# Kernel optimization log

Measured on AMD Instinct MI355X. Metric: run time of the kernel, lower is better.

## Reference

```python
import jax, jax.numpy as jnp
import numpy as np

N_BATCHES = 32
N_LABELS = 100


def setup_inputs() -> dict:
    key = jax.random.key(0)
    ks = jax.random.split(key, 7)
    N, D, P = 16384, 2048, 256
    x = jax.random.normal(ks[0], (N, D), dtype=jnp.float32)
    label = jax.random.randint(ks[1], (N,), 0, N_LABELS, dtype=jnp.int64)
    label_batch = jnp.sort(jax.random.randint(ks[2], (N,), 0, N_BATCHES, dtype=jnp.int64))
    W1_w = jax.random.normal(ks[3], (P, D), dtype=jnp.float32) * 0.02
    W1_b = jax.random.normal(ks[4], (P,), dtype=jnp.float32) * 0.02
    W2_w = jax.random.normal(ks[5], (P, D), dtype=jnp.float32) * 0.02
    W2_b = jax.random.normal(ks[6], (P,), dtype=jnp.float32) * 0.02
    return {"x": x, "label": label, "label_batch": label_batch,
            "W1_w": W1_w, "W1_b": W1_b, "W2_w": W2_w, "W2_b": W2_b}


def _loo_diff_label_mean(x, label, label_batch):
    # For each sample i: mean of x over {j : label_batch[j]==label_batch[i] and label[j]!=label[i]}.
    # Rows with no such j are zero (torch code's `continue`). x is detached in the original.
    N = x.shape[0]
    xs = jax.lax.stop_gradient(x)
    seg = label_batch * N_LABELS + label                      # combined (group,label) key
    n_seg = N_BATCHES * N_LABELS
    ones = jnp.ones((N,), dtype=x.dtype)
    sum_bl = jax.ops.segment_sum(xs, seg, num_segments=n_seg)            # [n_seg, D]
    cnt_bl = jax.ops.segment_sum(ones, seg, num_segments=n_seg)          # [n_seg]
    sum_b = jax.ops.segment_sum(xs, label_batch, num_segments=N_BATCHES)  # [NB, D]
    cnt_b = jax.ops.segment_sum(ones, label_batch, num_segments=N_BATCHES)
    diff_sum = sum_b[label_batch] - sum_bl[seg]               # [N, D]
    diff_cnt = cnt_b[label_batch] - cnt_bl[seg]               # [N]
    safe = jnp.maximum(diff_cnt, 1.0)
    mean = diff_sum / safe[:, None]
    return jnp.where((diff_cnt > 0)[:, None], mean, jnp.zeros_like(mean))


def reference(x, label, label_batch, W1_w, W1_b, W2_w, W2_b):
    calc_mean = _loo_diff_label_mean(x, label, label_batch)   # detached aggregate
    return x @ W1_w.T + W1_b + calc_mean @ W2_w.T + W2_b      # W1(x) + W2(mean)
```

## Files before the change

### kernel.cpp

```cpp
#include <hip/hip_runtime.h>
#include <cstdint>

#define N_SAMPLES 16384
#define DIM 2048
#define PDIM 256
#define NB 32
#define NL 100
#define NSEG (NB * NL)

typedef float floatx4 __attribute__((ext_vector_type(4)));
typedef __bf16 bf16x8 __attribute__((ext_vector_type(8)));

__device__ __forceinline__ unsigned short f32_to_bf16(float f) {
    unsigned int u = __float_as_uint(f);
    u += 0x7fffu + ((u >> 16) & 1u);
    return (unsigned short)(u >> 16);
}
__device__ __forceinline__ unsigned int pack_bf16x2(float a, float b) {
    return (unsigned int)f32_to_bf16(a) | ((unsigned int)f32_to_bf16(b) << 16);
}

__global__ __launch_bounds__(256) void prep_kernel(
    const float* __restrict__ W1w, const float* __restrict__ W1b,
    const float* __restrict__ W2w, const float* __restrict__ W2b,
    const int* __restrict__ label, const int* __restrict__ lbatch,
    unsigned short* __restrict__ W1bf, unsigned short* __restrict__ W2bf,
    float* __restrict__ bias, int* __restrict__ seg,
    int* __restrict__ hist, float* __restrict__ MW2)
{
    int i = blockIdx.x * 256 + threadIdx.x;
    W1bf[i] = f32_to_bf16(W1w[i]);
    W2bf[i] = f32_to_bf16(W2w[i]);
    if (i < PDIM) bias[i] = W1b[i] + W2b[i];
    if (i < N_SAMPLES) seg[i] = lbatch[i] * NL + label[i];
    if (i < NSEG) hist[i] = 0;
    if (i < NSEG * PDIM / 2) ((float2*)MW2)[i] = make_float2(0.f, 0.f);
}

__global__ __launch_bounds__(256) void hist_kernel(
    const int* __restrict__ seg, int* __restrict__ hist)
{
    int i = blockIdx.x * 256 + threadIdx.x;
    atomicAdd(&hist[seg[i]], 1);
}

#define SCAN_BPT 13
__global__ __launch_bounds__(256) void scan_kernel(
    const int* __restrict__ hist, int* __restrict__ offs, int* __restrict__ cursor)
{
    __shared__ int ps[256];
    const int t = threadIdx.x;
    int local = 0;
    #pragma unroll
    for (int k = 0; k < SCAN_BPT; ++k) {
        int bin = t * SCAN_BPT + k;
        if (bin < NSEG) local += hist[bin];
    }
    ps[t] = local;
    __syncthreads();
    for (int d = 1; d < 256; d <<= 1) {
        int v = (t >= d) ? ps[t - d] : 0;
        __syncthreads();
        ps[t] += v;
        __syncthreads();
    }
    int run = ps[t] - local;
    #pragma unroll
    for (int k = 0; k < SCAN_BPT; ++k) {
        int bin = t * SCAN_BPT + k;
        if (bin < NSEG) {
            offs[bin] = run;
            cursor[bin] = run;
            run += hist[bin];
        }
    }
    if (t == 255) offs[NSEG] = ps[255];
}

__global__ __launch_bounds__(256) void scatter_kernel(
    const int* __restrict__ seg, int* __restrict__ cursor, int* __restrict__ perm)
{
    int i = blockIdx.x * 256 + threadIdx.x;
    int pos = atomicAdd(&cursor[seg[i]], 1);
    perm[pos] = i;
}

__global__ __launch_bounds__(256) void segsum_kernel(
    const float* __restrict__ x, const int* __restrict__ perm,
    const int* __restrict__ offs,
    unsigned short* __restrict__ xb, float* __restrict__ sum_bl)
{
    const int tid = threadIdx.x;
    const int w = tid >> 6, lane = tid & 63;
    const int s = blockIdx.y * 4 + w;
    const int c = blockIdx.x * 512 + lane * 8;
    const int beg = offs[s], end = offs[s + 1];

    floatx4 sum0 = {0.f, 0.f, 0.f, 0.f};
    floatx4 sum1 = {0.f, 0.f, 0.f, 0.f};
    for (int base = beg; base < end; base += 64) {
        int p = (base + lane < end) ? perm[base + lane] : 0;
        const int n = min(end - base, 64);
        for (int j0 = 0; j0 < n; j0 += 8) {
            int rr[8];
            floatx4 v0[8], v1[8];
            #pragma unroll
            for (int j = 0; j < 8; ++j) {
                rr[j] = __shfl(p, min(j0 + j, n - 1));
                const float* px = &x[(size_t)rr[j] * DIM + c];
                v0[j] = *(const floatx4*)px;
                v1[j] = *(const floatx4*)(px + 4);
            }
            #pragma unroll
            for (int j = 0; j < 8; ++j) {
                if (j < n - j0) {
                    sum0 += v0[j];
                    sum1 += v1[j];
                    uint4 o;
                    o.x = pack_bf16x2(v0[j][0], v0[j][1]);
                    o.y = pack_bf16x2(v0[j][2], v0[j][3]);
                    o.z = pack_bf16x2(v1[j][0], v1[j][1]);
                    o.w = pack_bf16x2(v1[j][2], v1[j][3]);
                    *(uint4*)&xb[(size_t)rr[j] * DIM + c] = o;
                }
            }
        }
    }
    *(floatx4*)&sum_bl[(size_t)s * DIM + c] = sum0;
    *(floatx4*)&sum_bl[(size_t)s * DIM + c + 4] = sum1;
}

__global__ __launch_bounds__(256) void meanm_kernel(
    const float* __restrict__ sum_bl, const int* __restrict__ offs,
    unsigned short* __restrict__ Mb)
{
    __shared__ float acc[NL][256];
    const int tid = threadIdx.x;
    const int b = blockIdx.y;
    const int c = blockIdx.x * 256 + tid;

    float tot = 0.f;
    for (int l0 = 0; l0 < NL; l0 += 4) {
        float v[4];
        #pragma unroll
        for (int j = 0; j < 4; ++j)
            v[j] = sum_bl[(size_t)(b * NL + l0 + j) * DIM + c];
        #pragma unroll
        for (int j = 0; j < 4; ++j) { acc[l0 + j][tid] = v[j]; tot += v[j]; }
    }

    const int ob = offs[b * NL];
    const int cb = offs[(b + 1) * NL] - ob;
    for (int l = 0; l < NL; ++l) {
        int dc = cb - (offs[b * NL + l + 1] - offs[b * NL + l]);
        float m = (dc > 0) ? (tot - acc[l][tid]) / (float)dc : 0.f;
        Mb[(size_t)(b * NL + l) * DIM + c] = f32_to_bf16(m);
    }
}

template<int BM, int BN, int WR, int WC, bool FUSE, int KSPLIT>
__global__ __launch_bounds__(256) void gemm_bt_kernel(
    const unsigned short* __restrict__ A,
    const unsigned short* __restrict__ B,
    float* __restrict__ C,
    const float* __restrict__ bias,
    const float* __restrict__ add,
    const int* __restrict__ seg,
    int K)
{
    constexpr int SM = BM / WR, SN = BN / WC;
    constexpr int FM = SM / 16, FN = SN / 16;
    __shared__ __align__(16) unsigned short ldsA[BM * 32];
    __shared__ __align__(16) unsigned short ldsB[BN * 32];
    const int tid = threadIdx.x;
    const int lane = tid & 63;
    const int wave = tid >> 6;
    const int wr = wave / WC, wc = wave % WC;
    const int quad = lane >> 4, l15 = lane & 15;
    const int m0 = blockIdx.x * BM;
    const int n0 = blockIdx.y * BN;
    const int kpw = K / KSPLIT;
    const int k0 = blockIdx.z * kpw;
    const int srow = lane >> 2, schunk = lane & 3;

    floatx4 acc[FM][FN];
    #pragma unroll
    for (int i = 0; i < FM; ++i)
        #pragma unroll
        for (int j = 0; j < FN; ++j) acc[i][j] = (floatx4){0.f, 0.f, 0.f, 0.f};

    const unsigned short* Abase = A + (size_t)(m0 + srow) * K + schunk * 8;
    const unsigned short* Bbase = B + (size_t)(n0 + srow) * K + schunk * 8;

    for (int kk = k0; kk < k0 + kpw; kk += 32) {
        __syncthreads();
        #pragma unroll
        for (int ch = wave; ch < BM / 16; ch += 4)
            __builtin_amdgcn_global_load_lds(
                (const __attribute__((address_space(1))) void*)(Abase + (size_t)ch * 16 * K + kk),
                (__attribute__((address_space(3))) void*)&ldsA[ch * 16 * 32], 16, 0, 0);
        #pragma unroll
        for (int ch = wave; ch < BN / 16; ch += 4)
            __builtin_amdgcn_global_load_lds(
                (const __attribute__((address_space(1))) void*)(Bbase + (size_t)ch * 16 * K + kk),
                (__attribute__((address_space(3))) void*)&ldsB[ch * 16 * 32], 16, 0, 0);
        __syncthreads();

        bf16x8 af[FM], bfr[FN];
        #pragma unroll
        for (int mi = 0; mi < FM; ++mi)
            af[mi] = *(const bf16x8*)&ldsA[(wr * SM + mi * 16 + l15) * 32 + quad * 8];
        #pragma unroll
        for (int ni = 0; ni < FN; ++ni)
            bfr[ni] = *(const bf16x8*)&ldsB[(wc * SN + ni * 16 + l15) * 32 + quad * 8];
        #pragma unroll
        for (int mi = 0; mi < FM; ++mi)
            #pragma unroll
            for (int ni = 0; ni < FN; ++ni)
                acc[mi][ni] = __builtin_amdgcn_mfma_f32_16x16x32_bf16(
                    af[mi], bfr[ni], acc[mi][ni], 0, 0, 0);
    }

    #pragma unroll
    for (int mi = 0; mi < FM; ++mi) {
        const int rbase = m0 + wr * SM + mi * 16 + quad * 4;
        #pragma unroll
        for (int ni = 0; ni < FN; ++ni) {
            const int col = n0 + wc * SN + ni * 16 + l15;
            float bsum = 0.f;
            if constexpr (FUSE) bsum = bias[col];
            #pragma unroll
            for (int r = 0; r < 4; ++r) {
                const int row = rbase + r;
                float v = acc[mi][ni][r];
                if constexpr (FUSE) v += bsum + add[(size_t)seg[row] * PDIM + col];
                if constexpr (KSPLIT > 1)
                    atomicAdd(&C[(size_t)row * PDIM + col], v);
                else
                    C[(size_t)row * PDIM + col] = v;
            }
        }
    }
}

extern "C" void kernel_launch(void* const* d_in, const int* in_sizes, int n_in,
                              void* d_out, int out_size, void* d_ws, size_t ws_size,
                              hipStream_t stream)
{
    const float* x      = (const float*)d_in[0];
    const int*   label  = (const int*)d_in[1];
    const int*   lbatch = (const int*)d_in[2];
    const float* W1w    = (const float*)d_in[3];
    const float* W1b    = (const float*)d_in[4];
    const float* W2w    = (const float*)d_in[5];
    const float* W2b    = (const float*)d_in[6];
    float* out = (float*)d_out;

    char* ws = (char*)d_ws;
    size_t off = 0;
    auto alloc = [&](size_t bytes) {
        void* p = ws + off;
        off = (off + bytes + 255) & ~(size_t)255;
        return p;
    };
    unsigned short* xb   = (unsigned short*)alloc((size_t)N_SAMPLES * DIM * 2);
    unsigned short* Mb   = (unsigned short*)alloc((size_t)NSEG * DIM * 2);
    unsigned short* W1bf = (unsigned short*)alloc((size_t)PDIM * DIM * 2);
    unsigned short* W2bf = (unsigned short*)alloc((size_t)PDIM * DIM * 2);
    float* MW2    = (float*)alloc((size_t)NSEG * PDIM * 4);
    float* sum_bl = (float*)alloc((size_t)NSEG * DIM * 4);
    float* bias   = (float*)alloc(PDIM * 4);
    int*   seg    = (int*)alloc(N_SAMPLES * 4);
    int*   perm   = (int*)alloc(N_SAMPLES * 4);
    int*   hist   = (int*)alloc(NSEG * 4);
    int*   offs   = (int*)alloc((NSEG + 1) * 4);
    int*   cursor = (int*)alloc(NSEG * 4);

    prep_kernel<<<PDIM * DIM / 256, 256, 0, stream>>>(
        W1w, W1b, W2w, W2b, label, lbatch, W1bf, W2bf, bias, seg, hist, MW2);

    hist_kernel<<<N_SAMPLES / 256, 256, 0, stream>>>(seg, hist);
    scan_kernel<<<1, 256, 0, stream>>>(hist, offs, cursor);
    scatter_kernel<<<N_SAMPLES / 256, 256, 0, stream>>>(seg, cursor, perm);

    segsum_kernel<<<dim3(DIM / 512, NSEG / 4), 256, 0, stream>>>(
        x, perm, offs, xb, sum_bl);

    meanm_kernel<<<dim3(DIM / 256, NB), 256, 0, stream>>>(sum_bl, offs, Mb);

    gemm_bt_kernel<32, 256, 1, 4, false, 2>
        <<<dim3(NSEG / 32, 1, 2), 256, 0, stream>>>(
        Mb, W2bf, MW2, nullptr, nullptr, nullptr, DIM);

    gemm_bt_kernel<64, 128, 2, 2, true, 1>
        <<<dim3(N_SAMPLES / 64, PDIM / 128), 256, 0, stream>>>(
        xb, W1bf, out, bias, MW2, seg, DIM);
}
```

Measured before the change: 317.7 us.

## Merge histogram/scan/scatter into one block and split-K the main GEMM

Result: slower. 379.7 us (+19.5%).

```diff
diff --git a/kernel.cpp b/kernel.cpp
--- a/kernel.cpp
+++ b/kernel.cpp
@@ -26,35 +26,39 @@
     const int* __restrict__ label, const int* __restrict__ lbatch,
     unsigned short* __restrict__ W1bf, unsigned short* __restrict__ W2bf,
     float* __restrict__ bias, int* __restrict__ seg,
-    int* __restrict__ hist, float* __restrict__ MW2)
+    float* __restrict__ MW2, float* __restrict__ out)
 {
     int i = blockIdx.x * 256 + threadIdx.x;
     W1bf[i] = f32_to_bf16(W1w[i]);
     W2bf[i] = f32_to_bf16(W2w[i]);
     if (i < PDIM) bias[i] = W1b[i] + W2b[i];
     if (i < N_SAMPLES) seg[i] = lbatch[i] * NL + label[i];
-    if (i < NSEG) hist[i] = 0;
     if (i < NSEG * PDIM / 2) ((float2*)MW2)[i] = make_float2(0.f, 0.f);
-}
-
-__global__ __launch_bounds__(256) void hist_kernel(
-    const int* __restrict__ seg, int* __restrict__ hist)
-{
-    int i = blockIdx.x * 256 + threadIdx.x;
-    atomicAdd(&hist[seg[i]], 1);
+    ((float4*)out)[i] = make_float4(0.f, 0.f, 0.f, 0.f);
+    ((float4*)out)[i + PDIM * DIM] = make_float4(0.f, 0.f, 0.f, 0.f);
 }
 
 #define SCAN_BPT 13
-__global__ __launch_bounds__(256) void scan_kernel(
-    const int* __restrict__ hist, int* __restrict__ offs, int* __restrict__ cursor)
-{
+__global__ __launch_bounds__(256) void sortseg_kernel(
+    const int* __restrict__ label, const int* __restrict__ lbatch,
+    int* __restrict__ offs, int* __restrict__ perm)
+{
+    __shared__ int lhist[NSEG];
+    __shared__ int lcur[NSEG];
     __shared__ int ps[256];
     const int t = threadIdx.x;
+
+    for (int i = t; i < NSEG; i += 256) lhist[i] = 0;
+    __syncthreads();
+    for (int i = t; i < N_SAMPLES; i += 256)
+        atomicAdd(&lhist[lbatch[i] * NL + label[i]], 1);
+    __syncthreads();
+
     int local = 0;
     #pragma unroll
     for (int k = 0; k < SCAN_BPT; ++k) {
         int bin = t * SCAN_BPT + k;
-        if (bin < NSEG) local += hist[bin];
+        if (bin < NSEG) local += lhist[bin];
     }
     ps[t] = local;
     __syncthreads();
@@ -70,19 +74,17 @@
         int bin = t * SCAN_BPT + k;
         if (bin < NSEG) {
             offs[bin] = run;
-            cursor[bin] = run;
-            run += hist[bin];
+            lcur[bin] = run;
+            run += lhist[bin];
         }
     }
     if (t == 255) offs[NSEG] = ps[255];
-}
-
-__global__ __launch_bounds__(256) void scatter_kernel(
-    const int* __restrict__ seg, int* __restrict__ cursor, int* __restrict__ perm)
-{
-    int i = blockIdx.x * 256 + threadIdx.x;
-    int pos = atomicAdd(&cursor[seg[i]], 1);
-    perm[pos] = i;
+    __syncthreads();
+    for (int i = t; i < N_SAMPLES; i += 256) {
+        int s = lbatch[i] * NL + label[i];
+        int pos = atomicAdd(&lcur[s], 1);
+        perm[pos] = i;
+    }
 }
 
 __global__ __launch_bounds__(256) void segsum_kernel(
@@ -149,8 +151,7 @@
         for (int j = 0; j < 4; ++j) { acc[l0 + j][tid] = v[j]; tot += v[j]; }
     }
 
-    const int ob = offs[b * NL];
-    const int cb = offs[(b + 1) * NL] - ob;
+    const int cb = offs[(b + 1) * NL] - offs[b * NL];
     for (int l = 0; l < NL; ++l) {
         int dc = cb - (offs[b * NL + l + 1] - offs[b * NL + l]);
         float m = (dc > 0) ? (tot - acc[l][tid]) / (float)dc : 0.f;
@@ -221,19 +222,19 @@
                     af[mi], bfr[ni], acc[mi][ni], 0, 0, 0);
     }
 
+    const bool do_fuse = FUSE && (KSPLIT == 1 || blockIdx.z == 0);
     #pragma unroll
     for (int mi = 0; mi < FM; ++mi) {
         const int rbase = m0 + wr * SM + mi * 16 + quad * 4;
         #pragma unroll
         for (int ni = 0; ni < FN; ++ni) {
             const int col = n0 + wc * SN + ni * 16 + l15;
-            float bsum = 0.f;
-            if constexpr (FUSE) bsum = bias[col];
+            float bsum = do_fuse ? bias[col] : 0.f;
             #pragma unroll
             for (int r = 0; r < 4; ++r) {
                 const int row = rbase + r;
                 float v = acc[mi][ni][r];
-                if constexpr (FUSE) v += bsum + add[(size_t)seg[row] * PDIM + col];
+                if (do_fuse) v += bsum + add[(size_t)seg[row] * PDIM + col];
                 if constexpr (KSPLIT > 1)
                     atomicAdd(&C[(size_t)row * PDIM + col], v);
                 else
@@ -272,16 +273,12 @@
     float* bias   = (float*)alloc(PDIM * 4);
     int*   seg    = (int*)alloc(N_SAMPLES * 4);
     int*   perm   = (int*)alloc(N_SAMPLES * 4);
-    int*   hist   = (int*)alloc(NSEG * 4);
     int*   offs   = (int*)alloc((NSEG + 1) * 4);
-    int*   cursor = (int*)alloc(NSEG * 4);
 
     prep_kernel<<<PDIM * DIM / 256, 256, 0, stream>>>(
-        W1w, W1b, W2w, W2b, label, lbatch, W1bf, W2bf, bias, seg, hist, MW2);
-
-    hist_kernel<<<N_SAMPLES / 256, 256, 0, stream>>>(seg, hist);
-    scan_kernel<<<1, 256, 0, stream>>>(hist, offs, cursor);
-    scatter_kernel<<<N_SAMPLES / 256, 256, 0, stream>>>(seg, cursor, perm);
+        W1w, W1b, W2w, W2b, label, lbatch, W1bf, W2bf, bias, seg, MW2, out);
+
+    sortseg_kernel<<<1, 256, 0, stream>>>(label, lbatch, offs, perm);
 
     segsum_kernel<<<dim3(DIM / 512, NSEG / 4), 256, 0, stream>>>(
         x, perm, offs, xb, sum_bl);
@@ -292,7 +289,7 @@
         <<<dim3(NSEG / 32, 1, 2), 256, 0, stream>>>(
         Mb, W2bf, MW2, nullptr, nullptr, nullptr, DIM);
 
-    gemm_bt_kernel<64, 128, 2, 2, true, 1>
-        <<<dim3(N_SAMPLES / 64, PDIM / 128), 256, 0, stream>>>(
+    gemm_bt_kernel<64, 256, 2, 2, true, 2>
+        <<<dim3(N_SAMPLES / 64, 1, 2), 256, 0, stream>>>(
         xb, W1bf, out, bias, MW2, seg, DIM);
 }
```
